# Kernel optimization log

Measured on AMD Instinct MI355X. Metric: run time of the kernel, lower is better.

The kernel has to match this reference:

```python
import jax, jax.numpy as jnp
import numpy as np

# Clause structure: 4 unary clauses and 4 binary (joined-space) clauses,
# each with 3 literals; first literal negated ('n' prefix).
U_IDX = np.array([[0, 1, 2], [3, 4, 5], [6, 7, 8], [9, 10, 11]], dtype=np.int32)
U_SIGNS = np.array([[-1.0, 1.0, 1.0]] * 4, dtype=np.float32)
# Joined matrix columns: [u[i1] (0..15), u[i2] (16..31), binary (32..35)]
B_IDX = np.array([[0, 16, 32], [1, 17, 33], [2, 18, 34], [3, 19, 35]], dtype=np.int32)
B_SIGNS = np.array([[-1.0, 1.0, 1.0]] * 4, dtype=np.float32)

N_NODES, N_UNARY = 50000, 16
N_EDGES, N_BINARY = 1600000, 4
INIT_W = 0.5


def setup_inputs() -> dict:
    key = jax.random.key(0)
    k1, k2, k3, k4 = jax.random.split(key, 4)
    unary = jax.random.normal(k1, (N_NODES, N_UNARY), dtype=jnp.float32)
    binary = jax.random.normal(k2, (N_EDGES, N_BINARY), dtype=jnp.float32)
    edge_index = jax.random.randint(k3, (2, N_EDGES), 0, N_NODES, dtype=jnp.int32)
    wu = jnp.full((4,), INIT_W, dtype=jnp.float32)  # learnable unary clause weights
    wb = jnp.full((4,), INIT_W, dtype=jnp.float32)  # learnable binary clause weights
    return {"unary": unary, "binary": binary, "wu": wu, "wb": wb, "edge_index": edge_index}


def _knowledge_enhancer(x, idx, signs, w):
    """x: [R, P]; idx/signs: [C, L]; w: [C]. Returns summed deltas [R, P]."""
    lit = x[:, idx] * signs                                    # [R, C, L] signed literals
    d = (w[:, None] * jax.nn.softmax(lit, axis=-1)) * signs    # [R, C, L] signed deltas
    return jnp.zeros_like(x).at[:, idx].add(d)                 # scatter-sum over clauses


def reference(unary, binary, wu, wb, edge_index):
    i1, i2 = edge_index[0], edge_index[1]
    P = unary.shape[1]
    # Unary knowledge enhancement
    u = unary + _knowledge_enhancer(unary, U_IDX, U_SIGNS, wu)
    # Join: per-edge [u[i1] | u[i2] | binary]
    joined = jnp.concatenate([u[i1], u[i2], binary], axis=1)   # [E, 2P+B]
    d = _knowledge_enhancer(joined, B_IDX, B_SIGNS, wb)        # [E, 2P+B]
    # GroupBy: scatter node blocks back, keep binary block
    n = unary.shape[0]
    delta_up = (jax.ops.segment_sum(d[:, :P], i1, num_segments=n)
                + jax.ops.segment_sum(d[:, P:2 * P], i2, num_segments=n))
    delta_bp = d[:, 2 * P:]
    # activation = identity (default)
    return u + delta_up, binary + delta_bp
```

## Files before the change

kernel.cpp:

```cpp
#include <hip/hip_runtime.h>
#include <hip/hip_bf16.h>

#define N_NODES 50000
#define N_UNARY 16
#define N_EDGES 1600000
#define N_BINARY 4

typedef float vfloat4 __attribute__((ext_vector_type(4)));

#define FP_SCALE 127.0f
#define FP_INV   (1.0f / 127.0f)

#define BUCKET_SHIFT 11
#define BUCKET_NODES 2048
#define N_BUCKETS 25
#define N_GROUPS 50
#define SEG_CAP 73728
#define N_CHUNKS 10

#define TAILS_STRIDE 16

#define SCAT_BLOCK 512
#define SCAT_RECS (2 * SCAT_BLOCK)

#define SEG_BYTES   ((size_t)N_GROUPS * SEG_CAP * 8)
#define TAILS_BYTES ((size_t)4096)
#define PART_BYTES  ((size_t)N_GROUPS * N_CHUNKS * BUCKET_NODES * 8)
#define UE_BYTES    ((size_t)N_NODES * 16)
#define WS_NEEDED   (SEG_BYTES + TAILS_BYTES + PART_BYTES + UE_BYTES)

__device__ inline void enhance_u4(const float x[6], float wu0, float wu1,
                                  float u[4]) {
    float l0 = -x[0], l1 = x[1], l2 = x[2];
    float m  = fmaxf(l0, fmaxf(l1, l2));
    float e0 = __expf(l0 - m), e1 = __expf(l1 - m), e2 = __expf(l2 - m);
    float inv = 1.0f / (e0 + e1 + e2);
    u[0] = x[0] - wu0 * e0 * inv;
    u[1] = x[1] + wu0 * e1 * inv;
    u[2] = x[2] + wu0 * e2 * inv;
    float l3 = -x[3], l4 = x[4], l5 = x[5];
    float m2 = fmaxf(l3, fmaxf(l4, l5));
    float f0 = __expf(l3 - m2), f1 = __expf(l4 - m2), f2 = __expf(l5 - m2);
    float inv2 = 1.0f / (f0 + f1 + f2);
    u[3] = x[3] - wu1 * f0 * inv2;
}

__device__ inline void edge_math(const float* unary, const float* binary,
                                 float wu0, float wu1, const float wc[4],
                                 int i1, int i2, int e,
                                 float s0[4], float s1[4],
                                 float* out_b) {
    const float4* u1p = (const float4*)(unary + (size_t)i1 * N_UNARY);
    const float4* u2p = (const float4*)(unary + (size_t)i2 * N_UNARY);
    float4 x1a = u1p[0], x1b = u1p[1];
    float4 x2a = u2p[0], x2b = u2p[1];
    float xa[6] = {x1a.x, x1a.y, x1a.z, x1a.w, x1b.x, x1b.y};
    float xb[6] = {x2a.x, x2a.y, x2a.z, x2a.w, x2b.x, x2b.y};
    float a[4], b[4];
    enhance_u4(xa, wu0, wu1, a);
    enhance_u4(xb, wu0, wu1, b);

    vfloat4 bn = __builtin_nontemporal_load((const vfloat4*)binary + e);
    float bb[4] = {bn.x, bn.y, bn.z, bn.w};
    float ob[4];
#pragma unroll
    for (int c = 0; c < 4; ++c) {
        float l0 = -a[c], l1 = b[c], l2 = bb[c];
        float m  = fmaxf(l0, fmaxf(l1, l2));
        float e0 = __expf(l0 - m);
        float e1 = __expf(l1 - m);
        float e2 = __expf(l2 - m);
        float inv = 1.0f / (e0 + e1 + e2);
        s0[c] = e0 * inv;
        s1[c] = e1 * inv;
        ob[c] = bb[c] + wc[c] * e2 * inv;
    }
    vfloat4 obv = {ob[0], ob[1], ob[2], ob[3]};
    __builtin_nontemporal_store(obv, (vfloat4*)out_b + e);
}

__device__ inline unsigned long long make_rec(const float s[4], int local_id) {
    unsigned v0 = __float2uint_rn(s[0] * FP_SCALE);
    unsigned v1 = __float2uint_rn(s[1] * FP_SCALE);
    unsigned v2 = __float2uint_rn(s[2] * FP_SCALE);
    unsigned v3 = __float2uint_rn(s[3] * FP_SCALE);
    unsigned pl = v0 | (v1 << 7) | (v2 << 14) | (v3 << 21);
    return (unsigned long long)pl | ((unsigned long long)(unsigned)local_id << 28);
}

__device__ inline unsigned long long pack4_16(const float s[4]) {
    unsigned long long a = __float2uint_rn(s[0] * FP_SCALE);
    unsigned long long b = __float2uint_rn(s[1] * FP_SCALE);
    unsigned long long c = __float2uint_rn(s[2] * FP_SCALE);
    unsigned long long d = __float2uint_rn(s[3] * FP_SCALE);
    return a | (b << 16) | (c << 32) | (d << 48);
}

__global__ void __launch_bounds__(256)
kenn_pre_kernel(const float* __restrict__ unary,
                const float* __restrict__ wu,
                float4* __restrict__ ue,
                unsigned* __restrict__ tails) {
    int n = blockIdx.x * blockDim.x + threadIdx.x;
    if (n < N_GROUPS) tails[n * TAILS_STRIDE] = 0u;
    if (n >= N_NODES) return;
    const float4* up = (const float4*)(unary + (size_t)n * N_UNARY);
    float4 x0 = up[0], x1 = up[1];
    float x[6] = {x0.x, x0.y, x0.z, x0.w, x1.x, x1.y};
    float u[4];
    enhance_u4(x, wu[0], wu[1], u);
    ue[n] = make_float4(u[0], u[1], u[2], u[3]);
}

__global__ void __launch_bounds__(SCAT_BLOCK)
kenn_edge_scatter_kernel(const float4* __restrict__ ue,
                         const float* __restrict__ binary,
                         const float* __restrict__ wb,
                         const int* __restrict__ edge_index,
                         unsigned long long* __restrict__ segs,
                         unsigned* __restrict__ tails,
                         float* __restrict__ out_b) {
    __shared__ unsigned l_cnt[N_GROUPS];
    __shared__ unsigned l_pref[N_GROUPS];
    __shared__ unsigned l_gbase[N_GROUPS];
    __shared__ unsigned long long staged[SCAT_RECS];
    __shared__ unsigned char staged_g[SCAT_RECS];

    int tid = threadIdx.x;
    if (tid < N_GROUPS) l_cnt[tid] = 0;
    __syncthreads();

    int e = blockIdx.x * SCAT_BLOCK + tid;
    int i1 = __builtin_nontemporal_load(edge_index + e);
    int i2 = __builtin_nontemporal_load(edge_index + N_EDGES + e);

    float4 av = ue[i1];
    float4 bv = ue[i2];
    float a[4] = {av.x, av.y, av.z, av.w};
    float b[4] = {bv.x, bv.y, bv.z, bv.w};
    vfloat4 bn = __builtin_nontemporal_load((const vfloat4*)binary + e);
    float bb[4] = {bn.x, bn.y, bn.z, bn.w};
    float wc[4] = {wb[0], wb[1], wb[2], wb[3]};

    float s0[4], s1[4], ob[4];
#pragma unroll
    for (int c = 0; c < 4; ++c) {
        float l0 = -a[c], l1 = b[c], l2 = bb[c];
        float m  = fmaxf(l0, fmaxf(l1, l2));
        float e0 = __expf(l0 - m);
        float e1 = __expf(l1 - m);
        float e2 = __expf(l2 - m);
        float inv = 1.0f / (e0 + e1 + e2);
        s0[c] = e0 * inv;
        s1[c] = e1 * inv;
        ob[c] = bb[c] + wc[c] * e2 * inv;
    }
    vfloat4 obv = {ob[0], ob[1], ob[2], ob[3]};
    __builtin_nontemporal_store(obv, (vfloat4*)out_b + e);

    unsigned long long rec1 = make_rec(s0, i1 & (BUCKET_NODES - 1));
    unsigned long long rec2 = make_rec(s1, i2 & (BUCKET_NODES - 1));
    int g1 = i1 >> BUCKET_SHIFT;
    int g2 = N_BUCKETS + (i2 >> BUCKET_SHIFT);
    unsigned pos1 = atomicAdd(&l_cnt[g1], 1u);
    unsigned pos2 = atomicAdd(&l_cnt[g2], 1u);
    __syncthreads();

    if (tid < 64) {
        unsigned c = (tid < N_GROUPS) ? l_cnt[tid] : 0u;
        unsigned s = c;
#pragma unroll
        for (int off = 1; off < 64; off <<= 1) {
            unsigned o = __shfl_up(s, off, 64);
            if (tid >= off) s += o;
        }
        if (tid < N_GROUPS) l_pref[tid] = s - c;
    } else if (tid >= 64 && tid < 64 + N_GROUPS) {
        int g = tid - 64;
        unsigned c = l_cnt[g];
        l_gbase[g] = c ? atomicAdd(tails + g * TAILS_STRIDE, c) : 0u;
    }
    __syncthreads();

    unsigned p1 = l_pref[g1] + pos1;
    unsigned p2 = l_pref[g2] + pos2;
    staged[p1] = rec1;  staged_g[p1] = (unsigned char)g1;
    staged[p2] = rec2;  staged_g[p2] = (unsigned char)g2;
    __syncthreads();

#pragma unroll
    for (int k = 0; k < 2; ++k) {
        unsigned i = (unsigned)tid + k * SCAT_BLOCK;
        unsigned g = staged_g[i];
        unsigned long long rec = staged[i];
        unsigned p = l_gbase[g] + (i - l_pref[g]);
        if (p < SEG_CAP)
            __builtin_nontemporal_store(rec, segs + (size_t)g * SEG_CAP + p);
    }
}

__global__ void __launch_bounds__(512)
kenn_reduce_kernel(const unsigned long long* __restrict__ segs,
                   const unsigned* __restrict__ tails,
                   unsigned long long* __restrict__ partials) {
    __shared__ unsigned long long lacc[BUCKET_NODES];
    int chunk = blockIdx.x;
    int g     = blockIdx.y;
    int tid   = threadIdx.x;

    for (int i = tid; i < BUCKET_NODES; i += blockDim.x) lacc[i] = 0ull;
    __syncthreads();

    unsigned cnt = tails[g * TAILS_STRIDE];
    if (cnt > SEG_CAP) cnt = SEG_CAP;
    unsigned csz   = (cnt + N_CHUNKS - 1) / N_CHUNKS;
    unsigned start = chunk * csz;
    unsigned end   = start + csz;
    if (end > cnt) end = cnt;

    const unsigned long long* seg = segs + (size_t)g * SEG_CAP;
    for (unsigned i = start + tid; i < end; i += blockDim.x) {
        unsigned long long r = seg[i];
        unsigned id = (unsigned)(r >> 28) & (BUCKET_NODES - 1);
        unsigned pl = (unsigned)r & 0x0FFFFFFFu;
        unsigned long long exp =
            (unsigned long long)(pl & 127u) |
            ((unsigned long long)(pl & (127u << 7))  << 9)  |
            ((unsigned long long)(pl & (127u << 14)) << 18) |
            ((unsigned long long)(pl & (127u << 21)) << 27);
        atomicAdd(&lacc[id], exp);
    }
    __syncthreads();

    unsigned long long* dst =
        partials + ((size_t)g * N_CHUNKS + chunk) * BUCKET_NODES;
    for (int i = tid; i < BUCKET_NODES; i += blockDim.x)
        __builtin_nontemporal_store(lacc[i], dst + i);
}

__global__ void kenn_node_final_kernel(const float* __restrict__ unary,
                                       const float* __restrict__ wu,
                                       const float* __restrict__ wb,
                                       const unsigned long long* __restrict__ partials,
                                       const unsigned long long* __restrict__ accN,
                                       const unsigned long long* __restrict__ accP,
                                       int use_partials,
                                       float* __restrict__ out_u) {
    int node = blockIdx.x * blockDim.x + threadIdx.x;
    if (node >= N_NODES) return;

    const float4* up = (const float4*)(unary + (size_t)node * N_UNARY);
    float4 x0 = up[0], x1 = up[1], x2 = up[2], x3 = up[3];
    float x[16] = {x0.x, x0.y, x0.z, x0.w,
                   x1.x, x1.y, x1.z, x1.w,
                   x2.x, x2.y, x2.z, x2.w,
                   x3.x, x3.y, x3.z, x3.w};
    float wuc[4] = {wu[0], wu[1], wu[2], wu[3]};

    float y[16];
#pragma unroll
    for (int i = 0; i < 16; ++i) y[i] = x[i];

#pragma unroll
    for (int c = 0; c < 4; ++c) {
        float l0 = -x[3 * c + 0];
        float l1 =  x[3 * c + 1];
        float l2 =  x[3 * c + 2];
        float m  = fmaxf(l0, fmaxf(l1, l2));
        float e0 = __expf(l0 - m);
        float e1 = __expf(l1 - m);
        float e2 = __expf(l2 - m);
        float inv = 1.0f / (e0 + e1 + e2);
        y[3 * c + 0] -= wuc[c] * e0 * inv;
        y[3 * c + 1] += wuc[c] * e1 * inv;
        y[3 * c + 2] += wuc[c] * e2 * inv;
    }

    unsigned long long pn, pp;
    if (use_partials) {
        int bucket = node >> BUCKET_SHIFT;
        int local  = node & (BUCKET_NODES - 1);
        const unsigned long long* pN =
            partials + ((size_t)bucket * N_CHUNKS) * BUCKET_NODES + local;
        const unsigned long long* pP =
            partials + ((size_t)(N_BUCKETS + bucket) * N_CHUNKS) * BUCKET_NODES + local;
        pn = 0ull; pp = 0ull;
#pragma unroll
        for (int c = 0; c < N_CHUNKS; ++c) {
            pn += pN[(size_t)c * BUCKET_NODES];
            pp += pP[(size_t)c * BUCKET_NODES];
        }
    } else {
        pn = accN[node];
        pp = accP[node];
    }

    float wbc[4] = {wb[0], wb[1], wb[2], wb[3]};
    y[0] += wbc[0] * ((float)(int)((pp      ) & 0xffff) - (float)(int)((pn      ) & 0xffff)) * FP_INV;
    y[1] += wbc[1] * ((float)(int)((pp >> 16) & 0xffff) - (float)(int)((pn >> 16) & 0xffff)) * FP_INV;
    y[2] += wbc[2] * ((float)(int)((pp >> 32) & 0xffff) - (float)(int)((pn >> 32) & 0xffff)) * FP_INV;
    y[3] += wbc[3] * ((float)(int)((pp >> 48) & 0xffff) - (float)(int)((pn >> 48) & 0xffff)) * FP_INV;

    float4* op = (float4*)(out_u + (size_t)node * N_UNARY);
    op[0] = make_float4(y[0],  y[1],  y[2],  y[3]);
    op[1] = make_float4(y[4],  y[5],  y[6],  y[7]);
    op[2] = make_float4(y[8],  y[9],  y[10], y[11]);
    op[3] = make_float4(y[12], y[13], y[14], y[15]);
}

__global__ void kenn_edge_atomic_kernel(const float* __restrict__ unary,
                                        const float* __restrict__ binary,
                                        const float* __restrict__ wu,
                                        const float* __restrict__ wb,
                                        const int* __restrict__ edge_index,
                                        unsigned long long* __restrict__ accN,
                                        unsigned long long* __restrict__ accP,
                                        float* __restrict__ out_b) {
    int e = blockIdx.x * blockDim.x + threadIdx.x;
    if (e >= N_EDGES) return;
    int i1 = __builtin_nontemporal_load(edge_index + e);
    int i2 = __builtin_nontemporal_load(edge_index + N_EDGES + e);
    float wu0 = wu[0], wu1 = wu[1];
    float wc[4] = {wb[0], wb[1], wb[2], wb[3]};
    float s0[4], s1[4];
    edge_math(unary, binary, wu0, wu1, wc, i1, i2, e, s0, s1, out_b);
    atomicAdd(accN + i1, pack4_16(s0));
    atomicAdd(accP + i2, pack4_16(s1));
}

extern "C" void kernel_launch(void* const* d_in, const int* in_sizes, int n_in,
                              void* d_out, int out_size, void* d_ws, size_t ws_size,
                              hipStream_t stream) {
    const float* unary      = (const float*)d_in[0];
    const float* binary     = (const float*)d_in[1];
    const float* wu         = (const float*)d_in[2];
    const float* wb         = (const float*)d_in[3];
    const int*   edge_index = (const int*)d_in[4];

    float* out_u = (float*)d_out;
    float* out_b = (float*)d_out + (size_t)N_NODES * N_UNARY;

    if (ws_size >= WS_NEEDED) {
        unsigned long long* segs = (unsigned long long*)d_ws;
        unsigned* tails = (unsigned*)((char*)d_ws + SEG_BYTES);
        unsigned long long* partials =
            (unsigned long long*)((char*)d_ws + SEG_BYTES + TAILS_BYTES);
        float4* ue =
            (float4*)((char*)d_ws + SEG_BYTES + TAILS_BYTES + PART_BYTES);

        {
            dim3 grid((N_NODES + 255) / 256);
            kenn_pre_kernel<<<grid, dim3(256), 0, stream>>>(unary, wu, ue, tails);
        }
        {
            dim3 grid(N_EDGES / SCAT_BLOCK);
            kenn_edge_scatter_kernel<<<grid, dim3(SCAT_BLOCK), 0, stream>>>(
                ue, binary, wb, edge_index, segs, tails, out_b);
        }
        {
            dim3 grid(N_CHUNKS, N_GROUPS);
            kenn_reduce_kernel<<<grid, dim3(512), 0, stream>>>(
                segs, tails, partials);
        }
        {
            dim3 block(256);
            dim3 grid((N_NODES + 255) / 256);
            kenn_node_final_kernel<<<grid, block, 0, stream>>>(
                unary, wu, wb, partials, nullptr, nullptr, 1, out_u);
        }
    } else {
        unsigned long long* accN = (unsigned long long*)d_ws;
        unsigned long long* accP = accN + N_NODES;
        (void)hipMemsetAsync(accN, 0,
                             (size_t)N_NODES * 2 * sizeof(unsigned long long),
                             stream);
        {
            dim3 block(256);
            dim3 grid((N_EDGES + 255) / 256);
            kenn_edge_atomic_kernel<<<grid, block, 0, stream>>>(
                unary, binary, wu, wb, edge_index, accN, accP, out_b);
        }
        {
            dim3 block(256);
            dim3 grid((N_NODES + 255) / 256);
            kenn_node_final_kernel<<<grid, block, 0, stream>>>(
                unary, wu, wb, nullptr, accN, accP, 0, out_u);
        }
    }
}
```

Baseline: 172.6 us.

## Replace bucketed segment scatter and reduce with direct 64-bit global atomics

The bucketed record scatter plus per-bucket LDS reduction pipeline is replaced by per-edge 64-bit global atomicAdds of packed fixed-point contributions into node accumulators. Alternating blocks write to two replica accumulator sets to spread atomic contention. The final node kernel sums the replicas. This drops one kernel, the staging shared memory and the partials traffic, but now depends on global atomic throughput under random node indices.

After: 234.7 us. 36.0% more time.

```diff
diff --git a/kernel.cpp b/kernel.cpp
--- a/kernel.cpp
+++ b/kernel.cpp
@@ -1,5 +1,4 @@
 #include <hip/hip_runtime.h>
-#include <hip/hip_bf16.h>
 
 #define N_NODES 50000
 #define N_UNARY 16
@@ -11,23 +10,12 @@
 #define FP_SCALE 127.0f
 #define FP_INV   (1.0f / 127.0f)
 
-#define BUCKET_SHIFT 11
-#define BUCKET_NODES 2048
-#define N_BUCKETS 25
-#define N_GROUPS 50
-#define SEG_CAP 73728
-#define N_CHUNKS 10
-
-#define TAILS_STRIDE 16
-
-#define SCAT_BLOCK 512
-#define SCAT_RECS (2 * SCAT_BLOCK)
-
-#define SEG_BYTES   ((size_t)N_GROUPS * SEG_CAP * 8)
-#define TAILS_BYTES ((size_t)4096)
-#define PART_BYTES  ((size_t)N_GROUPS * N_CHUNKS * BUCKET_NODES * 8)
-#define UE_BYTES    ((size_t)N_NODES * 16)
-#define WS_NEEDED   (SEG_BYTES + TAILS_BYTES + PART_BYTES + UE_BYTES)
+#define ACC_BYTES ((size_t)4 * N_NODES * 8)
+#define UE_BYTES  ((size_t)N_NODES * 16)
+#define WS_NEEDED (ACC_BYTES + UE_BYTES)
+#define WS_MIN    ((size_t)2 * N_NODES * 8)
+
+#define EDGE_BLOCK 256
 
 __device__ inline void enhance_u4(const float x[6], float wu0, float wu1,
                                   float u[4]) {
@@ -45,21 +33,23 @@
     u[3] = x[3] - wu1 * f0 * inv2;
 }
 
-__device__ inline void edge_math(const float* unary, const float* binary,
-                                 float wu0, float wu1, const float wc[4],
-                                 int i1, int i2, int e,
+__device__ inline unsigned long long pack4_16(const float s[4]) {
+    unsigned long long a = __float2uint_rn(s[0] * FP_SCALE);
+    unsigned long long b = __float2uint_rn(s[1] * FP_SCALE);
+    unsigned long long c = __float2uint_rn(s[2] * FP_SCALE);
+    unsigned long long d = __float2uint_rn(s[3] * FP_SCALE);
+    return a | (b << 16) | (c << 32) | (d << 48);
+}
+
+__device__ inline void edge_core(const float4* __restrict__ ue,
+                                 const float* __restrict__ binary,
+                                 const float wc[4], int i1, int i2, int e,
                                  float s0[4], float s1[4],
-                                 float* out_b) {
-    const float4* u1p = (const float4*)(unary + (size_t)i1 * N_UNARY);
-    const float4* u2p = (const float4*)(unary + (size_t)i2 * N_UNARY);
-    float4 x1a = u1p[0], x1b = u1p[1];
-    float4 x2a = u2p[0], x2b = u2p[1];
-    float xa[6] = {x1a.x, x1a.y, x1a.z, x1a.w, x1b.x, x1b.y};
-    float xb[6] = {x2a.x, x2a.y, x2a.z, x2a.w, x2b.x, x2b.y};
-    float a[4], b[4];
-    enhance_u4(xa, wu0, wu1, a);
-    enhance_u4(xb, wu0, wu1, b);
-
+                                 float* __restrict__ out_b) {
+    float4 av = ue[i1];
+    float4 bv = ue[i2];
+    float a[4] = {av.x, av.y, av.z, av.w};
+    float b[4] = {bv.x, bv.y, bv.z, bv.w};
     vfloat4 bn = __builtin_nontemporal_load((const vfloat4*)binary + e);
     float bb[4] = {bn.x, bn.y, bn.z, bn.w};
     float ob[4];
@@ -79,31 +69,17 @@
     __builtin_nontemporal_store(obv, (vfloat4*)out_b + e);
 }
 
-__device__ inline unsigned long long make_rec(const float s[4], int local_id) {
-    unsigned v0 = __float2uint_rn(s[0] * FP_SCALE);
-    unsigned v1 = __float2uint_rn(s[1] * FP_SCALE);
-    unsigned v2 = __float2uint_rn(s[2] * FP_SCALE);
-    unsigned v3 = __float2uint_rn(s[3] * FP_SCALE);
-    unsigned pl = v0 | (v1 << 7) | (v2 << 14) | (v3 << 21);
-    return (unsigned long long)pl | ((unsigned long long)(unsigned)local_id << 28);
-}
-
-__device__ inline unsigned long long pack4_16(const float s[4]) {
-    unsigned long long a = __float2uint_rn(s[0] * FP_SCALE);
-    unsigned long long b = __float2uint_rn(s[1] * FP_SCALE);
-    unsigned long long c = __float2uint_rn(s[2] * FP_SCALE);
-    unsigned long long d = __float2uint_rn(s[3] * FP_SCALE);
-    return a | (b << 16) | (c << 32) | (d << 48);
-}
-
 __global__ void __launch_bounds__(256)
 kenn_pre_kernel(const float* __restrict__ unary,
                 const float* __restrict__ wu,
                 float4* __restrict__ ue,
-                unsigned* __restrict__ tails) {
-    int n = blockIdx.x * blockDim.x + threadIdx.x;
-    if (n < N_GROUPS) tails[n * TAILS_STRIDE] = 0u;
+                unsigned long long* __restrict__ acc) {
+    int n = blockIdx.x * 256 + threadIdx.x;
     if (n >= N_NODES) return;
+    acc[n] = 0ull;
+    acc[(size_t)N_NODES + n] = 0ull;
+    acc[(size_t)2 * N_NODES + n] = 0ull;
+    acc[(size_t)3 * N_NODES + n] = 0ull;
     const float4* up = (const float4*)(unary + (size_t)n * N_UNARY);
     float4 x0 = up[0], x1 = up[1];
     float x[6] = {x0.x, x0.y, x0.z, x0.w, x1.x, x1.y};
@@ -112,141 +88,33 @@
     ue[n] = make_float4(u[0], u[1], u[2], u[3]);
 }
 
-__global__ void __launch_bounds__(SCAT_BLOCK)
-kenn_edge_scatter_kernel(const float4* __restrict__ ue,
-                         const float* __restrict__ binary,
-                         const float* __restrict__ wb,
-                         const int* __restrict__ edge_index,
-                         unsigned long long* __restrict__ segs,
-                         unsigned* __restrict__ tails,
-                         float* __restrict__ out_b) {
-    __shared__ unsigned l_cnt[N_GROUPS];
-    __shared__ unsigned l_pref[N_GROUPS];
-    __shared__ unsigned l_gbase[N_GROUPS];
-    __shared__ unsigned long long staged[SCAT_RECS];
-    __shared__ unsigned char staged_g[SCAT_RECS];
-
-    int tid = threadIdx.x;
-    if (tid < N_GROUPS) l_cnt[tid] = 0;
-    __syncthreads();
-
-    int e = blockIdx.x * SCAT_BLOCK + tid;
+__global__ void __launch_bounds__(EDGE_BLOCK)
+kenn_edge_kernel(const float4* __restrict__ ue,
+                 const float* __restrict__ binary,
+                 const float* __restrict__ wb,
+                 const int* __restrict__ edge_index,
+                 unsigned long long* __restrict__ acc,
+                 float* __restrict__ out_b) {
+    int e = blockIdx.x * EDGE_BLOCK + threadIdx.x;
+    if (e >= N_EDGES) return;
     int i1 = __builtin_nontemporal_load(edge_index + e);
     int i2 = __builtin_nontemporal_load(edge_index + N_EDGES + e);
-
-    float4 av = ue[i1];
-    float4 bv = ue[i2];
-    float a[4] = {av.x, av.y, av.z, av.w};
-    float b[4] = {bv.x, bv.y, bv.z, bv.w};
-    vfloat4 bn = __builtin_nontemporal_load((const vfloat4*)binary + e);
-    float bb[4] = {bn.x, bn.y, bn.z, bn.w};
     float wc[4] = {wb[0], wb[1], wb[2], wb[3]};
-
-    float s0[4], s1[4], ob[4];
-#pragma unroll
-    for (int c = 0; c < 4; ++c) {
-        float l0 = -a[c], l1 = b[c], l2 = bb[c];
-        float m  = fmaxf(l0, fmaxf(l1, l2));
-        float e0 = __expf(l0 - m);
-        float e1 = __expf(l1 - m);
-        float e2 = __expf(l2 - m);
-        float inv = 1.0f / (e0 + e1 + e2);
-        s0[c] = e0 * inv;
-        s1[c] = e1 * inv;
-        ob[c] = bb[c] + wc[c] * e2 * inv;
-    }
-    vfloat4 obv = {ob[0], ob[1], ob[2], ob[3]};
-    __builtin_nontemporal_store(obv, (vfloat4*)out_b + e);
-
-    unsigned long long rec1 = make_rec(s0, i1 & (BUCKET_NODES - 1));
-    unsigned long long rec2 = make_rec(s1, i2 & (BUCKET_NODES - 1));
-    int g1 = i1 >> BUCKET_SHIFT;
-    int g2 = N_BUCKETS + (i2 >> BUCKET_SHIFT);
-    unsigned pos1 = atomicAdd(&l_cnt[g1], 1u);
-    unsigned pos2 = atomicAdd(&l_cnt[g2], 1u);
-    __syncthreads();
-
-    if (tid < 64) {
-        unsigned c = (tid < N_GROUPS) ? l_cnt[tid] : 0u;
-        unsigned s = c;
-#pragma unroll
-        for (int off = 1; off < 64; off <<= 1) {
-            unsigned o = __shfl_up(s, off, 64);
-            if (tid >= off) s += o;
-        }
-        if (tid < N_GROUPS) l_pref[tid] = s - c;
-    } else if (tid >= 64 && tid < 64 + N_GROUPS) {
-        int g = tid - 64;
-        unsigned c = l_cnt[g];
-        l_gbase[g] = c ? atomicAdd(tails + g * TAILS_STRIDE, c) : 0u;
-    }
-    __syncthreads();
-
-    unsigned p1 = l_pref[g1] + pos1;
-    unsigned p2 = l_pref[g2] + pos2;
-    staged[p1] = rec1;  staged_g[p1] = (unsigned char)g1;
-    staged[p2] = rec2;  staged_g[p2] = (unsigned char)g2;
-    __syncthreads();
-
-#pragma unroll
-    for (int k = 0; k < 2; ++k) {
-        unsigned i = (unsigned)tid + k * SCAT_BLOCK;
-        unsigned g = staged_g[i];
-        unsigned long long rec = staged[i];
-        unsigned p = l_gbase[g] + (i - l_pref[g]);
-        if (p < SEG_CAP)
-            __builtin_nontemporal_store(rec, segs + (size_t)g * SEG_CAP + p);
-    }
-}
-
-__global__ void __launch_bounds__(512)
-kenn_reduce_kernel(const unsigned long long* __restrict__ segs,
-                   const unsigned* __restrict__ tails,
-                   unsigned long long* __restrict__ partials) {
-    __shared__ unsigned long long lacc[BUCKET_NODES];
-    int chunk = blockIdx.x;
-    int g     = blockIdx.y;
-    int tid   = threadIdx.x;
-
-    for (int i = tid; i < BUCKET_NODES; i += blockDim.x) lacc[i] = 0ull;
-    __syncthreads();
-
-    unsigned cnt = tails[g * TAILS_STRIDE];
-    if (cnt > SEG_CAP) cnt = SEG_CAP;
-    unsigned csz   = (cnt + N_CHUNKS - 1) / N_CHUNKS;
-    unsigned start = chunk * csz;
-    unsigned end   = start + csz;
-    if (end > cnt) end = cnt;
-
-    const unsigned long long* seg = segs + (size_t)g * SEG_CAP;
-    for (unsigned i = start + tid; i < end; i += blockDim.x) {
-        unsigned long long r = seg[i];
-        unsigned id = (unsigned)(r >> 28) & (BUCKET_NODES - 1);
-        unsigned pl = (unsigned)r & 0x0FFFFFFFu;
-        unsigned long long exp =
-            (unsigned long long)(pl & 127u) |
-            ((unsigned long long)(pl & (127u << 7))  << 9)  |
-            ((unsigned long long)(pl & (127u << 14)) << 18) |
-            ((unsigned long long)(pl & (127u << 21)) << 27);
-        atomicAdd(&lacc[id], exp);
-    }
-    __syncthreads();
-
-    unsigned long long* dst =
-        partials + ((size_t)g * N_CHUNKS + chunk) * BUCKET_NODES;
-    for (int i = tid; i < BUCKET_NODES; i += blockDim.x)
-        __builtin_nontemporal_store(lacc[i], dst + i);
-}
-
-__global__ void kenn_node_final_kernel(const float* __restrict__ unary,
-                                       const float* __restrict__ wu,
-                                       const float* __restrict__ wb,
-                                       const unsigned long long* __restrict__ partials,
-                                       const unsigned long long* __restrict__ accN,
-                                       const unsigned long long* __restrict__ accP,
-                                       int use_partials,
-                                       float* __restrict__ out_u) {
-    int node = blockIdx.x * blockDim.x + threadIdx.x;
+    float s0[4], s1[4];
+    edge_core(ue, binary, wc, i1, i2, e, s0, s1, out_b);
+    unsigned long long* a = acc + ((blockIdx.x & 1) ? (size_t)2 * N_NODES : 0);
+    atomicAdd(a + i1, pack4_16(s0));
+    atomicAdd(a + (size_t)N_NODES + i2, pack4_16(s1));
+}
+
+__global__ void __launch_bounds__(256)
+kenn_node_final_kernel(const float* __restrict__ unary,
+                       const float* __restrict__ wu,
+                       const float* __restrict__ wb,
+                       const unsigned long long* __restrict__ acc,
+                       int two_replicas,
+                       float* __restrict__ out_u) {
+    int node = blockIdx.x * 256 + threadIdx.x;
     if (node >= N_NODES) return;
 
     const float4* up = (const float4*)(unary + (size_t)node * N_UNARY);
@@ -276,23 +144,11 @@
         y[3 * c + 2] += wuc[c] * e2 * inv;
     }
 
-    unsigned long long pn, pp;
-    if (use_partials) {
-        int bucket = node >> BUCKET_SHIFT;
-        int local  = node & (BUCKET_NODES - 1);
-        const unsigned long long* pN =
-            partials + ((size_t)bucket * N_CHUNKS) * BUCKET_NODES + local;
-        const unsigned long long* pP =
-            partials + ((size_t)(N_BUCKETS + bucket) * N_CHUNKS) * BUCKET_NODES + local;
-        pn = 0ull; pp = 0ull;
-#pragma unroll
-        for (int c = 0; c < N_CHUNKS; ++c) {
-            pn += pN[(size_t)c * BUCKET_NODES];
-            pp += pP[(size_t)c * BUCKET_NODES];
-        }
-    } else {
-        pn = accN[node];
-        pp = accP[node];
+    unsigned long long pn = acc[node];
+    unsigned long long pp = acc[(size_t)N_NODES + node];
+    if (two_replicas) {
+        pn += acc[(size_t)2 * N_NODES + node];
+        pp += acc[(size_t)3 * N_NODES + node];
     }
 
     float wbc[4] = {wb[0], wb[1], wb[2], wb[3]};
@@ -308,24 +164,50 @@
     op[3] = make_float4(y[12], y[13], y[14], y[15]);
 }
 
-__global__ void kenn_edge_atomic_kernel(const float* __restrict__ unary,
-                                        const float* __restrict__ binary,
-                                        const float* __restrict__ wu,
-                                        const float* __restrict__ wb,
-                                        const int* __restrict__ edge_index,
-                                        unsigned long long* __restrict__ accN,
-                                        unsigned long long* __restrict__ accP,
-                                        float* __restrict__ out_b) {
+__global__ void kenn_edge_atomic_noue_kernel(const float* __restrict__ unary,
+                                             const float* __restrict__ binary,
+                                             const float* __restrict__ wu,
+                                             const float* __restrict__ wb,
+                                             const int* __restrict__ edge_index,
+                                             unsigned long long* __restrict__ acc,
+                                             float* __restrict__ out_b) {
     int e = blockIdx.x * blockDim.x + threadIdx.x;
     if (e >= N_EDGES) return;
     int i1 = __builtin_nontemporal_load(edge_index + e);
     int i2 = __builtin_nontemporal_load(edge_index + N_EDGES + e);
     float wu0 = wu[0], wu1 = wu[1];
     float wc[4] = {wb[0], wb[1], wb[2], wb[3]};
-    float s0[4], s1[4];
-    edge_math(unary, binary, wu0, wu1, wc, i1, i2, e, s0, s1, out_b);
-    atomicAdd(accN + i1, pack4_16(s0));
-    atomicAdd(accP + i2, pack4_16(s1));
+
+    const float4* u1p = (const float4*)(unary + (size_t)i1 * N_UNARY);
+    const float4* u2p = (const float4*)(unary + (size_t)i2 * N_UNARY);
+    float4 x1a = u1p[0], x1b = u1p[1];
+    float4 x2a = u2p[0], x2b = u2p[1];
+    float xa[6] = {x1a.x, x1a.y, x1a.z, x1a.w, x1b.x, x1b.y};
+    float xb[6] = {x2a.x, x2a.y, x2a.z, x2a.w, x2b.x, x2b.y};
+    float a[4], b[4];
+    enhance_u4(xa, wu0, wu1, a);
+    enhance_u4(xb, wu0, wu1, b);
+
+    vfloat4 bn = __builtin_nontemporal_load((const vfloat4*)binary + e);
+    float bb[4] = {bn.x, bn.y, bn.z, bn.w};
+    float s0[4], s1[4], ob[4];
+#pragma unroll
+    for (int c = 0; c < 4; ++c) {
+        float l0 = -a[c], l1 = b[c], l2 = bb[c];
+        float m  = fmaxf(l0, fmaxf(l1, l2));
+        float e0 = __expf(l0 - m);
+        float e1 = __expf(l1 - m);
+        float e2 = __expf(l2 - m);
+        float inv = 1.0f / (e0 + e1 + e2);
+        s0[c] = e0 * inv;
+        s1[c] = e1 * inv;
+        ob[c] = bb[c] + wc[c] * e2 * inv;
+    }
+    vfloat4 obv = {ob[0], ob[1], ob[2], ob[3]};
+    __builtin_nontemporal_store(obv, (vfloat4*)out_b + e);
+
+    atomicAdd(acc + i1, pack4_16(s0));
+    atomicAdd(acc + (size_t)N_NODES + i2, pack4_16(s1));
 }
 
 extern "C" void kernel_launch(void* const* d_in, const int* in_sizes, int n_in,
@@ -341,50 +223,36 @@
     float* out_b = (float*)d_out + (size_t)N_NODES * N_UNARY;
 
     if (ws_size >= WS_NEEDED) {
-        unsigned long long* segs = (unsigned long long*)d_ws;
-        unsigned* tails = (unsigned*)((char*)d_ws + SEG_BYTES);
-        unsigned long long* partials =
-            (unsigned long long*)((char*)d_ws + SEG_BYTES + TAILS_BYTES);
-        float4* ue =
-            (float4*)((char*)d_ws + SEG_BYTES + TAILS_BYTES + PART_BYTES);
+        unsigned long long* acc = (unsigned long long*)d_ws;
+        float4* ue = (float4*)((char*)d_ws + ACC_BYTES);
 
         {
             dim3 grid((N_NODES + 255) / 256);
-            kenn_pre_kernel<<<grid, dim3(256), 0, stream>>>(unary, wu, ue, tails);
-        }
-        {
-            dim3 grid(N_EDGES / SCAT_BLOCK);
-            kenn_edge_scatter_kernel<<<grid, dim3(SCAT_BLOCK), 0, stream>>>(
-                ue, binary, wb, edge_index, segs, tails, out_b);
-        }
-        {
-            dim3 grid(N_CHUNKS, N_GROUPS);
-            kenn_reduce_kernel<<<grid, dim3(512), 0, stream>>>(
-                segs, tails, partials);
-        }
-        {
-            dim3 block(256);
+            kenn_pre_kernel<<<grid, dim3(256), 0, stream>>>(unary, wu, ue, acc);
+        }
+        {
+            dim3 grid((N_EDGES + EDGE_BLOCK - 1) / EDGE_BLOCK);
+            kenn_edge_kernel<<<grid, dim3(EDGE_BLOCK), 0, stream>>>(
+                ue, binary, wb, edge_index, acc, out_b);
+        }
+        {
             dim3 grid((N_NODES + 255) / 256);
-            kenn_node_final_kernel<<<grid, block, 0, stream>>>(
-                unary, wu, wb, partials, nullptr, nullptr, 1, out_u);
+            kenn_node_final_kernel<<<grid, dim3(256), 0, stream>>>(
+                unary, wu, wb, acc, 1, out_u);
         }
     } else {
-        unsigned long long* accN = (unsigned long long*)d_ws;
-        unsigned long long* accP = accN + N_NODES;
-        (void)hipMemsetAsync(accN, 0,
-                             (size_t)N_NODES * 2 * sizeof(unsigned long long),
-                             stream);
+        unsigned long long* acc = (unsigned long long*)d_ws;
+        (void)hipMemsetAsync(acc, 0, WS_MIN, stream);
         {
             dim3 block(256);
             dim3 grid((N_EDGES + 255) / 256);
-            kenn_edge_atomic_kernel<<<grid, block, 0, stream>>>(
-                unary, binary, wu, wb, edge_index, accN, accP, out_b);
-        }
-        {
-            dim3 block(256);
+            kenn_edge_atomic_noue_kernel<<<grid, block, 0, stream>>>(
+                unary, binary, wu, wb, edge_index, acc, out_b);
+        }
+        {
             dim3 grid((N_NODES + 255) / 256);
-            kenn_node_final_kernel<<<grid, block, 0, stream>>>(
-                unary, wu, wb, nullptr, accN, accP, 0, out_u);
-        }
-    }
-}
+            kenn_node_final_kernel<<<grid, dim3(256), 0, stream>>>(
+                unary, wu, wb, acc, 0, out_u);
+        }
+    }
+}
```
